# Performance work log

Hardware: AMD Instinct MI355X
Metric: run time of the kernel (lower is better)

The kernel has to match this reference:

```python
import jax, jax.numpy as jnp
import numpy as np

N = 50000   # nodes
E = 800000  # edges
F = 128     # input features
H = 128     # hidden channels
G = 64      # graphs in batch
C = 10      # classes
L_HID = 3   # residual hidden GCN blocks
EPS = 1e-5  # BatchNorm eps


def setup_inputs() -> dict:
    key = jax.random.key(0)
    ks = jax.random.split(key, 10)
    sc = lambda k, s: (jax.random.normal(k, s, jnp.float32) * 0.05)
    x = jax.random.normal(ks[0], (N, F), jnp.float32)
    edge_index = jax.random.randint(ks[1], (2, E), 0, N, dtype=jnp.int32)
    batch = jnp.sort(jax.random.randint(ks[2], (N,), 0, G, dtype=jnp.int32))
    return {
        "x": x, "edge_index": edge_index, "batch": batch,
        # initial GCN block
        "W0": sc(ks[3], (F, H)), "b0": jnp.zeros(H, jnp.float32),
        "g0": jnp.ones(H, jnp.float32), "be0": jnp.zeros(H, jnp.float32),
        # 3 residual GCN blocks (stacked)
        "Wh": sc(ks[4], (L_HID, H, H)), "bh": jnp.zeros((L_HID, H), jnp.float32),
        "gh": jnp.ones((L_HID, H), jnp.float32), "beh": jnp.zeros((L_HID, H), jnp.float32),
        "Rh": sc(ks[5], (L_HID, H, H)),  # residual Linear (no bias)
        # MLP head: Linear(H,H)+ReLU, Linear(H,C)
        "mW1": sc(ks[6], (H, H)), "mb1": jnp.zeros(H, jnp.float32),
        "mW2": sc(ks[7], (H, C)), "mb2": jnp.zeros(C, jnp.float32),
    }


def _gcn_norm(edge_index, n):
    # add self-loops + symmetric normalization, as in PyG GCNConv
    loop = jnp.arange(n, dtype=edge_index.dtype)
    src = jnp.concatenate([edge_index[0], loop])
    dst = jnp.concatenate([edge_index[1], loop])
    deg = jax.ops.segment_sum(jnp.ones_like(dst, jnp.float32), dst, num_segments=n)
    dinv = jnp.where(deg > 0, jax.lax.rsqrt(deg), 0.0)
    coef = dinv[src] * dinv[dst]  # [E+N]
    return src, dst, coef


def _gcn_conv(x, W, b, src, dst, coef, n):
    h = x @ W                                   # [N, H] linear first (PyG order)
    msg = h[src] * coef[:, None]                # gather + normalize  [E+N, H]
    agg = jax.ops.segment_sum(msg, dst, num_segments=n)  # scatter-add [N, H]
    return agg + b


def _bn_relu(h, gamma, beta):
    # BatchNorm1d in eval mode with running_mean=0, running_var=1
    inv = jax.lax.rsqrt(jnp.asarray(1.0 + EPS, h.dtype))
    return jax.nn.relu(h * inv * gamma + beta)  # dropout is identity in eval


def reference(x, edge_index, batch, W0, b0, g0, be0, Wh, bh, gh, beh, Rh, mW1, mb1, mW2, mb2):
    n = x.shape[0]
    src, dst, coef = _gcn_norm(edge_index, n)
    # initial block (no residual)
    h = _bn_relu(_gcn_conv(x, W0, b0, src, dst, coef, n), g0, be0)
    # residual hidden blocks
    for i in range(Wh.shape[0]):
        c = _gcn_conv(h, Wh[i], bh[i], src, dst, coef, n) + h @ Rh[i]
        h = _bn_relu(c, gh[i], beh[i])
    # global max pool over graphs in the batch
    pooled = jax.ops.segment_max(h, batch, num_segments=G)  # [G, H]
    # MLP head
    z = jax.nn.relu(pooled @ mW1 + mb1)
    return z @ mW2 + mb2  # [G, C]
```

## Files before the change

### kernel.cpp

```cpp
#include <hip/hip_runtime.h>
#include <cstdint>
#include <cstddef>

#define NN 50000
#define NE 800000
#define NEPAD (NE + 3 * NN)
#define HID 128
#define NGRAPH 64
#define NCLASS 10
#define LHID 3

#define ROWBLK 3125
#define ROWBLK_PAD 3128
#define GEMM_GRID 782
#define FILL_GRID 3125
#define FRONT_A 3125
#define FRONT_B 56
#define FRONT_GRID (FRONT_A + FRONT_B + 3125)

static constexpr float BN_INV = 0.9999950000374996f;

typedef __attribute__((ext_vector_type(8))) __bf16 bf16x8;
typedef __attribute__((ext_vector_type(4))) float floatx4;


__device__ __forceinline__ unsigned int f32_to_bf16_rne(float f) {
    unsigned int u = __float_as_uint(f);
    return (u + 0x7FFFu + ((u >> 16) & 1u)) >> 16;
}
__device__ __forceinline__ float bf16_to_f32(unsigned int h) {
    return __uint_as_float(h << 16);
}
__device__ __forceinline__ void split2(float a, float b, unsigned int& hi,
                                       unsigned int& lo) {
    unsigned int h0 = f32_to_bf16_rne(a), h1 = f32_to_bf16_rne(b);
    unsigned int l0 = f32_to_bf16_rne(a - bf16_to_f32(h0));
    unsigned int l1 = f32_to_bf16_rne(b - bf16_to_f32(h1));
    hi = h0 | (h1 << 16);
    lo = l0 | (l1 << 16);
}

__device__ __forceinline__ void gl2lds16(const void* g, void* l) {
    __builtin_amdgcn_global_load_lds((__attribute__((address_space(1))) void*)g,
                                     (__attribute__((address_space(3))) void*)l,
                                     16, 0, 0);
}


__global__ void k_front(const float* __restrict__ x, unsigned short* __restrict__ xH,
                        unsigned short* __restrict__ xL,
                        const float* __restrict__ W0, const float* __restrict__ Wh,
                        const float* __restrict__ Rh, unsigned short* __restrict__ bH,
                        unsigned short* __restrict__ bL,
                        const int* __restrict__ ei, int* __restrict__ deg,
                        int* __restrict__ eslot) {
    const int b = blockIdx.x;
    const int tid = threadIdx.x;
    if (b < FRONT_A) {
        int u = b * 256 + tid;
        int lane = u & 63;
        int blk = u >> 6;
        int kblk = blk & 3;
        int rowBlock = blk >> 2;
        int m = rowBlock * 16 + (lane & 15);
        int k = kblk * 32 + (lane >> 4) * 8;
        const float4* p = (const float4*)&x[(size_t)m * 128 + k];
        float4 v0 = p[0];
        float4 v1 = p[1];
        float vals[8] = {v0.x, v0.y, v0.z, v0.w, v1.x, v1.y, v1.z, v1.w};
        union { unsigned int i[4]; uint4 v; } H, L;
#pragma unroll
        for (int j = 0; j < 4; ++j) split2(vals[2 * j], vals[2 * j + 1], H.i[j], L.i[j]);
        *(uint4*)&xH[(size_t)u * 8] = H.v;
        *(uint4*)&xL[(size_t)u * 8] = L.v;
    } else if (b < FRONT_A + FRONT_B) {
        int cb = b - FRONT_A;
        int mat = cb >> 3;
        const float* src = (mat == 0) ? W0
                         : (mat <= 3) ? (Wh + (size_t)(mat - 1) * 16384)
                                      : (Rh + (size_t)(mat - 4) * 16384);
        int u = (cb & 7) * 256 + tid;
        int lane = u & 63;
        int blk = u >> 6;
        int kblk = blk & 3;
        int nb = blk >> 2;
        int n = nb * 16 + (lane & 15);
        int k = kblk * 32 + (lane >> 4) * 8;
        union { unsigned int i[4]; uint4 v; } H, L;
#pragma unroll
        for (int j = 0; j < 4; ++j) {
            float a = src[(size_t)(k + 2 * j) * 128 + n];
            float c = src[(size_t)(k + 2 * j + 1) * 128 + n];
            split2(a, c, H.i[j], L.i[j]);
        }
        size_t base = (size_t)mat * 16384 + (size_t)u * 8;
        *(uint4*)&bH[base] = H.v;
        *(uint4*)&bL[base] = L.v;
    } else {
        int e = (b - FRONT_A - FRONT_B) * 256 + tid;
        int d = ei[NE + e];
        eslot[e] = atomicAdd(&deg[d], 1);
    }
}


__global__ void k_scan1(const int* __restrict__ deg, float* __restrict__ dinv,
                        int* __restrict__ bsum) {
    __shared__ int s[256];
    int i = blockIdx.x * 256 + threadIdx.x;
    int d = (i < NN) ? deg[i] : 0;
    if (i < NN) dinv[i] = rsqrtf((float)(d + 1));
    s[threadIdx.x] = (d + 3) & ~3;
    __syncthreads();
    for (int o = 128; o > 0; o >>= 1) {
        if (threadIdx.x < o) s[threadIdx.x] += s[threadIdx.x + o];
        __syncthreads();
    }
    if (threadIdx.x == 0) bsum[blockIdx.x] = s[0];
}


__global__ void k_scan3(const int* __restrict__ deg, const int* __restrict__ bsum,
                        int* __restrict__ rowptr, int* __restrict__ col,
                        float* __restrict__ cfv) {
    __shared__ int s[256];
    __shared__ int offS;
    const int bid = blockIdx.x;
    s[threadIdx.x] = (threadIdx.x < bid) ? bsum[threadIdx.x] : 0;
    __syncthreads();
    for (int o = 128; o > 0; o >>= 1) {
        if (threadIdx.x < o) s[threadIdx.x] += s[threadIdx.x + o];
        __syncthreads();
    }
    if (threadIdx.x == 0) offS = s[0];
    __syncthreads();
    const int off = offS;
    __syncthreads();
    int i = bid * 256 + threadIdx.x;
    int d = (i < NN) ? deg[i] : 0;
    int v = (d + 3) & ~3;
    s[threadIdx.x] = v;
    __syncthreads();
    for (int o = 1; o < 256; o <<= 1) {
        int tv = (threadIdx.x >= o) ? s[threadIdx.x - o] : 0;
        __syncthreads();
        s[threadIdx.x] += tv;
        __syncthreads();
    }
    if (i < NN) {
        int rp = off + s[threadIdx.x] - v;
        rowptr[i] = rp;
        for (int p = rp + d; p < rp + v; ++p) { col[p] = 0; cfv[p] = 0.f; }
    }
}


template <int NB, bool FILL>
__global__ __launch_bounds__(256, 3) void k_gemm_mfma(
    const unsigned short* __restrict__ Ahi, const unsigned short* __restrict__ Alo,
    const unsigned short* __restrict__ B1hi, const unsigned short* __restrict__ B1lo,
    const unsigned short* __restrict__ B2hi, const unsigned short* __restrict__ B2lo,
    float* __restrict__ C1, float* __restrict__ C2,
    const int* __restrict__ ei, const int* __restrict__ rowptr,
    const int* __restrict__ eslot, const float* __restrict__ dinv,
    int* __restrict__ col, float* __restrict__ cfv) {
    __shared__ unsigned short lds[(1 + 2 * NB) * 4096];
    if (FILL && blockIdx.x >= GEMM_GRID) {
        int e = (blockIdx.x - GEMM_GRID) * 256 + threadIdx.x;
        int s = ei[e];
        int d = ei[NE + e];
        int p = rowptr[d] + eslot[e];
        col[p] = s;
        cfv[p] = dinv[s];
        return;
    }
    unsigned short* AhiS = lds;
    unsigned short* AloS = lds + 2048;
    unsigned short* B1hiS = lds + 4096;
    unsigned short* B1loS = lds + 8192;
    unsigned short* B2hiS = lds + 12288;
    unsigned short* B2loS = lds + 16384;

    const int tid = threadIdx.x;
    const int wave = tid >> 6;
    const int lane = tid & 63;
    const int wm = wave & 1;
    const int wn = wave >> 1;
    const int rb0 = blockIdx.x * 4;

    floatx4 acc1[2][4], acc2[2][4];
    floatx4 zero = {0.f, 0.f, 0.f, 0.f};
#pragma unroll
    for (int i = 0; i < 2; ++i)
#pragma unroll
        for (int j = 0; j < 4; ++j) { acc1[i][j] = zero; if (NB == 2) acc2[i][j] = zero; }

    for (int kc = 0; kc < 4; ++kc) {
        const int nit = (NB == 2) ? 10 : 6;
#pragma unroll
        for (int it = 0; it < nit; ++it) {
            int i = it * 4 + wave;
            const unsigned short* src;
            unsigned short* dst;
            if (i < 4)       { src = Ahi  + ((size_t)(rb0 + i) * 4 + kc) * 512;       dst = AhiS  + i * 512; }
            else if (i < 8)  { int rb = i - 4;  src = Alo  + ((size_t)(rb0 + rb) * 4 + kc) * 512; dst = AloS  + rb * 512; }
            else if (i < 16) { int nb = i - 8;  src = B1hi + ((size_t)nb * 4 + kc) * 512;         dst = B1hiS + nb * 512; }
            else if (i < 24) { int nb = i - 16; src = B1lo + ((size_t)nb * 4 + kc) * 512;         dst = B1loS + nb * 512; }
            else if (i < 32) { int nb = i - 24; src = B2hi + ((size_t)nb * 4 + kc) * 512;         dst = B2hiS + nb * 512; }
            else             { int nb = i - 32; src = B2lo + ((size_t)nb * 4 + kc) * 512;         dst = B2loS + nb * 512; }
            gl2lds16(src + (size_t)lane * 8, dst);
        }
        __syncthreads();

        bf16x8 aH[2], aL[2], bH[4], bL[4];
#pragma unroll
        for (int t = 0; t < 2; ++t)
            aH[t] = *(const bf16x8*)(AhiS + (wm * 2 + t) * 512 + lane * 8);
#pragma unroll
        for (int t = 0; t < 4; ++t)
            bH[t] = *(const bf16x8*)(B1hiS + (wn * 4 + t) * 512 + lane * 8);
#pragma unroll
        for (int tm = 0; tm < 2; ++tm)
#pragma unroll
            for (int tn = 0; tn < 4; ++tn)
                acc1[tm][tn] = __builtin_amdgcn_mfma_f32_16x16x32_bf16(
                    aH[tm], bH[tn], acc1[tm][tn], 0, 0, 0);
#pragma unroll
        for (int t = 0; t < 4; ++t)
            bL[t] = *(const bf16x8*)(B1loS + (wn * 4 + t) * 512 + lane * 8);
#pragma unroll
        for (int tm = 0; tm < 2; ++tm)
#pragma unroll
            for (int tn = 0; tn < 4; ++tn)
                acc1[tm][tn] = __builtin_amdgcn_mfma_f32_16x16x32_bf16(
                    aH[tm], bL[tn], acc1[tm][tn], 0, 0, 0);
#pragma unroll
        for (int t = 0; t < 2; ++t)
            aL[t] = *(const bf16x8*)(AloS + (wm * 2 + t) * 512 + lane * 8);
#pragma unroll
        for (int tm = 0; tm < 2; ++tm)
#pragma unroll
            for (int tn = 0; tn < 4; ++tn)
                acc1[tm][tn] = __builtin_amdgcn_mfma_f32_16x16x32_bf16(
                    aL[tm], bH[tn], acc1[tm][tn], 0, 0, 0);
        if (NB == 2) {
#pragma unroll
            for (int t = 0; t < 4; ++t)
                bH[t] = *(const bf16x8*)(B2hiS + (wn * 4 + t) * 512 + lane * 8);
#pragma unroll
            for (int tm = 0; tm < 2; ++tm)
#pragma unroll
                for (int tn = 0; tn < 4; ++tn)
                    acc2[tm][tn] = __builtin_amdgcn_mfma_f32_16x16x32_bf16(
                        aH[tm], bH[tn], acc2[tm][tn], 0, 0, 0);
#pragma unroll
            for (int tm = 0; tm < 2; ++tm)
#pragma unroll
                for (int tn = 0; tn < 4; ++tn)
                    acc2[tm][tn] = __builtin_amdgcn_mfma_f32_16x16x32_bf16(
                        aL[tm], bH[tn], acc2[tm][tn], 0, 0, 0);
#pragma unroll
            for (int t = 0; t < 4; ++t)
                bL[t] = *(const bf16x8*)(B2loS + (wn * 4 + t) * 512 + lane * 8);
#pragma unroll
            for (int tm = 0; tm < 2; ++tm)
#pragma unroll
                for (int tn = 0; tn < 4; ++tn)
                    acc2[tm][tn] = __builtin_amdgcn_mfma_f32_16x16x32_bf16(
                        aH[tm], bL[tn], acc2[tm][tn], 0, 0, 0);
        }
        __syncthreads();
    }

    const int quad = lane >> 4;
    const int col0 = lane & 15;
    const int rowBase = blockIdx.x * 64 + wm * 32;
#pragma unroll
    for (int tm = 0; tm < 2; ++tm) {
#pragma unroll
        for (int tn = 0; tn < 4; ++tn) {
            int c = wn * 64 + tn * 16 + col0;
#pragma unroll
            for (int r = 0; r < 4; ++r) {
                int row = rowBase + tm * 16 + quad * 4 + r;
                if (row < NN) {
                    C1[(size_t)row * 128 + c] = acc1[tm][tn][r];
                    if (NB == 2) C2[(size_t)row * 128 + c] = acc2[tm][tn][r];
                }
            }
        }
    }
}


template <bool RES, bool LAST>
__global__ __launch_bounds__(256) void k_spmm(const float* __restrict__ t,
                                              const float* __restrict__ r,
                                              const int* __restrict__ rowptr,
                                              const int* __restrict__ deg,
                                              const int* __restrict__ col,
                                              const float* __restrict__ cfv,
                                              const float* __restrict__ dinv,
                                              const float* __restrict__ bias,
                                              const float* __restrict__ gamma,
                                              const float* __restrict__ beta,
                                              unsigned short* __restrict__ hHi,
                                              unsigned short* __restrict__ hLo,
                                              const int* __restrict__ batch,
                                              float* __restrict__ pooled) {
    __shared__ unsigned short shH[16][136];
    __shared__ unsigned short shL[16][136];
    const int lane = threadIdx.x & 63;
    const int wave = threadIdx.x >> 6;
    const int f = lane * 2;
    const float2 bv = *(const float2*)&bias[f];
    const float2 gv = *(const float2*)&gamma[f];
    const float2 ev = *(const float2*)&beta[f];

    int curg = -1;
    float mx = 0.f, my = 0.f;

#pragma unroll 1
    for (int i = 0; i < 4; ++i) {
        const int nl = wave * 4 + i;
        const int node = blockIdx.x * 16 + nl;
        const int start = rowptr[node];
        const int cnt4 = (deg[node] + 3) >> 2;
        float ax = 0.f, ay = 0.f;
#pragma unroll 2
        for (int q = 0; q < cnt4; ++q) {
            int4 cs = *(const int4*)&col[start + q * 4];
            float4 wv = *(const float4*)&cfv[start + q * 4];
            float2 v0 = *(const float2*)&t[(size_t)cs.x * 128 + f];
            float2 v1 = *(const float2*)&t[(size_t)cs.y * 128 + f];
            float2 v2 = *(const float2*)&t[(size_t)cs.z * 128 + f];
            float2 v3 = *(const float2*)&t[(size_t)cs.w * 128 + f];
            ax = fmaf(wv.x, v0.x, ax); ay = fmaf(wv.x, v0.y, ay);
            ax = fmaf(wv.y, v1.x, ax); ay = fmaf(wv.y, v1.y, ay);
            ax = fmaf(wv.z, v2.x, ax); ay = fmaf(wv.z, v2.y, ay);
            ax = fmaf(wv.w, v3.x, ax); ay = fmaf(wv.w, v3.y, ay);
        }
        const float di = dinv[node];
        const float dii = di * di;
        float2 tv = *(const float2*)&t[(size_t)node * 128 + f];
        float cx = di * ax + dii * tv.x + bv.x;
        float cy = di * ay + dii * tv.y + bv.y;
        if (RES) {
            float2 rv = *(const float2*)&r[(size_t)node * 128 + f];
            cx += rv.x;
            cy += rv.y;
        }
        float ox = fmaxf(cx * (BN_INV * gv.x) + ev.x, 0.f);
        float oy = fmaxf(cy * (BN_INV * gv.y) + ev.y, 0.f);
        if (LAST) {
            int g = batch[node];
            if (g != curg) {
                if (curg >= 0) {
                    atomicMax((unsigned int*)&pooled[curg * 128 + f], __float_as_uint(mx));
                    atomicMax((unsigned int*)&pooled[curg * 128 + f + 1], __float_as_uint(my));
                }
                curg = g; mx = ox; my = oy;
            } else {
                mx = fmaxf(mx, ox);
                my = fmaxf(my, oy);
            }
        } else {
            unsigned int H, L;
            split2(ox, oy, H, L);
            ((unsigned int*)&shH[nl][0])[lane] = H;
            ((unsigned int*)&shL[nl][0])[lane] = L;
        }
    }

    if (LAST) {
        if (curg >= 0) {
            atomicMax((unsigned int*)&pooled[curg * 128 + f], __float_as_uint(mx));
            atomicMax((unsigned int*)&pooled[curg * 128 + f + 1], __float_as_uint(my));
        }
        return;
    }
    __syncthreads();

    const int u = threadIdx.x >> 6;
    const int l = threadIdx.x & 63;
    const int m = l & 15;
    const int kg = l >> 4;
    uint4 H4 = *(const uint4*)&shH[m][u * 32 + kg * 8];
    uint4 L4 = *(const uint4*)&shL[m][u * 32 + kg * 8];
    ((uint4*)hHi)[((size_t)blockIdx.x * 4 + u) * 64 + l] = H4;
    ((uint4*)hLo)[((size_t)blockIdx.x * 4 + u) * 64 + l] = L4;
}


__global__ void k_head(const float* __restrict__ pooled, const float* __restrict__ mW1,
                       const float* __restrict__ mb1, const float* __restrict__ mW2,
                       const float* __restrict__ mb2, float* __restrict__ out) {
    __shared__ float p[128];
    __shared__ float z[128];
    int g = blockIdx.x;
    int j = threadIdx.x;
    p[j] = pooled[g * 128 + j];
    __syncthreads();
    float a = mb1[j];
#pragma unroll 8
    for (int k = 0; k < 128; ++k) a += p[k] * mW1[k * 128 + j];
    z[j] = fmaxf(a, 0.f);
    __syncthreads();
    if (j < NCLASS) {
        float o = mb2[j];
#pragma unroll 8
        for (int k = 0; k < 128; ++k) o += z[k] * mW2[k * NCLASS + j];
        out[g * NCLASS + j] = o;
    }
}


extern "C" void kernel_launch(void* const* d_in, const int* in_sizes, int n_in,
                              void* d_out, int out_size, void* d_ws, size_t ws_size,
                              hipStream_t stream) {
    const float* x   = (const float*)d_in[0];
    const int*   ei  = (const int*)d_in[1];
    const int* batch = (const int*)d_in[2];
    const float* W0  = (const float*)d_in[3];
    const float* b0  = (const float*)d_in[4];
    const float* g0  = (const float*)d_in[5];
    const float* be0 = (const float*)d_in[6];
    const float* Wh  = (const float*)d_in[7];
    const float* bh  = (const float*)d_in[8];
    const float* gh  = (const float*)d_in[9];
    const float* beh = (const float*)d_in[10];
    const float* Rh  = (const float*)d_in[11];
    const float* mW1 = (const float*)d_in[12];
    const float* mb1 = (const float*)d_in[13];
    const float* mW2 = (const float*)d_in[14];
    const float* mb2 = (const float*)d_in[15];
    float* out = (float*)d_out;

    char* ws = (char*)d_ws;
    size_t off = 0;
    auto alloc = [&](size_t bytes) -> void* {
        void* p = ws + off;
        off += (bytes + 255) & ~(size_t)255;
        return p;
    };
    int*   deg    = (int*)alloc((size_t)NN * 4);
    float* pooled = (float*)alloc((size_t)NGRAPH * HID * 4);
    size_t zspan = (size_t)((char*)pooled - (char*)deg) + (size_t)NGRAPH * HID * 4;
    int*   rowptr = (int*)alloc((size_t)NN * 4);
    float* dinv   = (float*)alloc((size_t)NN * 4);
    int*   bsum   = (int*)alloc(256 * 4);
    int*   eslot  = (int*)alloc((size_t)NE * 4);
    int*   col    = (int*)alloc((size_t)NEPAD * 4);
    float* cfv    = (float*)alloc((size_t)NEPAD * 4);
    float* t      = (float*)alloc((size_t)NN * HID * 4);
    float* rbuf   = (float*)alloc((size_t)NN * HID * 4);
    const size_t ASZ = (size_t)ROWBLK_PAD * 4 * 512;
    unsigned short* xH = (unsigned short*)alloc(ASZ * 2);
    unsigned short* xL = (unsigned short*)alloc(ASZ * 2);
    unsigned short* hH0 = (unsigned short*)alloc(ASZ * 2);
    unsigned short* hL0 = (unsigned short*)alloc(ASZ * 2);
    unsigned short* hH1 = (unsigned short*)alloc(ASZ * 2);
    unsigned short* hL1 = (unsigned short*)alloc(ASZ * 2);
    unsigned short* bH = (unsigned short*)alloc((size_t)7 * 16384 * 2);
    unsigned short* bL = (unsigned short*)alloc((size_t)7 * 16384 * 2);

    hipMemsetAsync(deg, 0, zspan, stream);

    k_front<<<FRONT_GRID, 256, 0, stream>>>(x, xH, xL, W0, Wh, Rh, bH, bL,
                                            ei, deg, eslot);
    k_scan1<<<(NN + 255) / 256, 256, 0, stream>>>(deg, dinv, bsum);
    k_scan3<<<(NN + 255) / 256, 256, 0, stream>>>(deg, bsum, rowptr, col, cfv);

    k_gemm_mfma<1, true><<<GEMM_GRID + FILL_GRID, 256, 0, stream>>>(
        xH, xL, bH, bL, nullptr, nullptr, t, nullptr,
        ei, rowptr, eslot, dinv, col, cfv);

    const int spmmGrid = NN / 16;
    k_spmm<false, false><<<spmmGrid, 256, 0, stream>>>(
        t, nullptr, rowptr, deg, col, cfv, dinv, b0, g0, be0, hH0, hL0,
        nullptr, nullptr);

    unsigned short* hh[2] = {hH0, hH1};
    unsigned short* hl[2] = {hL0, hL1};
    int cur = 0;
    for (int i = 0; i < LHID; ++i) {
        unsigned short* ih = hh[cur];
        unsigned short* il = hl[cur];
        unsigned short* oh = hh[cur ^ 1];
        unsigned short* ol = hl[cur ^ 1];
        const unsigned short* w1H = bH + (size_t)(1 + i) * 16384;
        const unsigned short* w1L = bL + (size_t)(1 + i) * 16384;
        const unsigned short* w2H = bH + (size_t)(4 + i) * 16384;
        const unsigned short* w2L = bL + (size_t)(4 + i) * 16384;
        k_gemm_mfma<2, false><<<GEMM_GRID, 256, 0, stream>>>(
            ih, il, w1H, w1L, w2H, w2L, t, rbuf,
            nullptr, nullptr, nullptr, nullptr, nullptr, nullptr);
        if (i < LHID - 1)
            k_spmm<true, false><<<spmmGrid, 256, 0, stream>>>(
                t, rbuf, rowptr, deg, col, cfv, dinv, bh + i * HID, gh + i * HID,
                beh + i * HID, oh, ol, nullptr, nullptr);
        else
            k_spmm<true, true><<<spmmGrid, 256, 0, stream>>>(
                t, rbuf, rowptr, deg, col, cfv, dinv, bh + i * HID, gh + i * HID,
                beh + i * HID, nullptr, nullptr, batch, pooled);
        cur ^= 1;
    }

    k_head<<<NGRAPH, 128, 0, stream>>>(pooled, mW1, mb1, mW2, mb2, out);
}
```

Baseline: 526.3 us.

## Fuse MLP head into last SpMM via last-block counter and uniform-graph pooling

Removes the separate head kernel launch: the last block of the final SpMM, found with an atomic completion counter, runs the MLP head over all pooled graphs. Blocks whose 16 nodes all belong to one graph first reduce their max in shared memory, so only wave 0 issues the atomicMax calls. The gather loop unroll also goes from 2 to 4. The cost is a serialized tail, where a single block computes the whole head, plus extra shared memory and sync barriers in the last SpMM.

```diff
diff --git a/kernel.cpp b/kernel.cpp
--- a/kernel.cpp
+++ b/kernel.cpp
@@ -307,9 +307,19 @@
                                               unsigned short* __restrict__ hHi,
                                               unsigned short* __restrict__ hLo,
                                               const int* __restrict__ batch,
-                                              float* __restrict__ pooled) {
+                                              float* __restrict__ pooled,
+                                              int* __restrict__ counter,
+                                              const float* __restrict__ mW1,
+                                              const float* __restrict__ mb1,
+                                              const float* __restrict__ mW2,
+                                              const float* __restrict__ mb2,
+                                              float* __restrict__ out) {
     __shared__ unsigned short shH[16][136];
     __shared__ unsigned short shL[16][136];
+    __shared__ float shP[4][64][2];
+    __shared__ float shPool[2][128];
+    __shared__ float shZ[2][128];
+    __shared__ int shDone;
     const int lane = threadIdx.x & 63;
     const int wave = threadIdx.x >> 6;
     const int f = lane * 2;
@@ -317,6 +327,8 @@
     const float2 gv = *(const float2*)&gamma[f];
     const float2 ev = *(const float2*)&beta[f];
 
+    bool uni = false;
+    if (LAST) uni = (batch[blockIdx.x * 16] == batch[blockIdx.x * 16 + 15]);
     int curg = -1;
     float mx = 0.f, my = 0.f;
 
@@ -327,7 +339,7 @@
         const int start = rowptr[node];
         const int cnt4 = (deg[node] + 3) >> 2;
         float ax = 0.f, ay = 0.f;
-#pragma unroll 2
+#pragma unroll 4
         for (int q = 0; q < cnt4; ++q) {
             int4 cs = *(const int4*)&col[start + q * 4];
             float4 wv = *(const float4*)&cfv[start + q * 4];
@@ -353,16 +365,21 @@
         float ox = fmaxf(cx * (BN_INV * gv.x) + ev.x, 0.f);
         float oy = fmaxf(cy * (BN_INV * gv.y) + ev.y, 0.f);
         if (LAST) {
-            int g = batch[node];
-            if (g != curg) {
-                if (curg >= 0) {
-                    atomicMax((unsigned int*)&pooled[curg * 128 + f], __float_as_uint(mx));
-                    atomicMax((unsigned int*)&pooled[curg * 128 + f + 1], __float_as_uint(my));
-                }
-                curg = g; mx = ox; my = oy;
-            } else {
+            if (uni) {
                 mx = fmaxf(mx, ox);
                 my = fmaxf(my, oy);
+            } else {
+                int g = batch[node];
+                if (g != curg) {
+                    if (curg >= 0) {
+                        atomicMax((unsigned int*)&pooled[curg * 128 + f], __float_as_uint(mx));
+                        atomicMax((unsigned int*)&pooled[curg * 128 + f + 1], __float_as_uint(my));
+                    }
+                    curg = g; mx = ox; my = oy;
+                } else {
+                    mx = fmaxf(mx, ox);
+                    my = fmaxf(my, oy);
+                }
             }
         } else {
             unsigned int H, L;
@@ -373,9 +390,54 @@
     }
 
     if (LAST) {
-        if (curg >= 0) {
-            atomicMax((unsigned int*)&pooled[curg * 128 + f], __float_as_uint(mx));
-            atomicMax((unsigned int*)&pooled[curg * 128 + f + 1], __float_as_uint(my));
+        if (uni) {
+            shP[wave][lane][0] = mx;
+            shP[wave][lane][1] = my;
+            __syncthreads();
+            if (wave == 0) {
+                int g = batch[blockIdx.x * 16];
+                float a = fmaxf(fmaxf(shP[0][lane][0], shP[1][lane][0]),
+                                fmaxf(shP[2][lane][0], shP[3][lane][0]));
+                float b = fmaxf(fmaxf(shP[0][lane][1], shP[1][lane][1]),
+                                fmaxf(shP[2][lane][1], shP[3][lane][1]));
+                atomicMax((unsigned int*)&pooled[g * 128 + f], __float_as_uint(a));
+                atomicMax((unsigned int*)&pooled[g * 128 + f + 1], __float_as_uint(b));
+            }
+        } else {
+            if (curg >= 0) {
+                atomicMax((unsigned int*)&pooled[curg * 128 + f], __float_as_uint(mx));
+                atomicMax((unsigned int*)&pooled[curg * 128 + f + 1], __float_as_uint(my));
+            }
+        }
+        __syncthreads();
+        if (threadIdx.x == 0) {
+            __threadfence();
+            shDone = atomicAdd(counter, 1);
+        }
+        __syncthreads();
+        if (shDone == (int)gridDim.x - 1) {
+            const int j = threadIdx.x & 127;
+            const int half = threadIdx.x >> 7;
+            for (int g0 = 0; g0 < NGRAPH; g0 += 2) {
+                int idx = threadIdx.x;
+                shPool[idx >> 7][idx & 127] = __uint_as_float(
+                    atomicMax((unsigned int*)&pooled[(g0 + (idx >> 7)) * 128 + (idx & 127)], 0u));
+                __syncthreads();
+                float a = mb1[j];
+#pragma unroll 8
+                for (int k = 0; k < 128; ++k)
+                    a = fmaf(shPool[half][k], mW1[k * 128 + j], a);
+                shZ[half][j] = fmaxf(a, 0.f);
+                __syncthreads();
+                if (j < NCLASS) {
+                    float o = mb2[j];
+#pragma unroll 8
+                    for (int k = 0; k < 128; ++k)
+                        o = fmaf(shZ[half][k], mW2[k * NCLASS + j], o);
+                    out[(g0 + half) * NCLASS + j] = o;
+                }
+                __syncthreads();
+            }
         }
         return;
     }
@@ -389,29 +451,6 @@
     uint4 L4 = *(const uint4*)&shL[m][u * 32 + kg * 8];
     ((uint4*)hHi)[((size_t)blockIdx.x * 4 + u) * 64 + l] = H4;
     ((uint4*)hLo)[((size_t)blockIdx.x * 4 + u) * 64 + l] = L4;
-}
-
-
-__global__ void k_head(const float* __restrict__ pooled, const float* __restrict__ mW1,
-                       const float* __restrict__ mb1, const float* __restrict__ mW2,
-                       const float* __restrict__ mb2, float* __restrict__ out) {
-    __shared__ float p[128];
-    __shared__ float z[128];
-    int g = blockIdx.x;
-    int j = threadIdx.x;
-    p[j] = pooled[g * 128 + j];
-    __syncthreads();
-    float a = mb1[j];
-#pragma unroll 8
-    for (int k = 0; k < 128; ++k) a += p[k] * mW1[k * 128 + j];
-    z[j] = fmaxf(a, 0.f);
-    __syncthreads();
-    if (j < NCLASS) {
-        float o = mb2[j];
-#pragma unroll 8
-        for (int k = 0; k < 128; ++k) o += z[k] * mW2[k * NCLASS + j];
-        out[g * NCLASS + j] = o;
-    }
 }
 
 
@@ -443,9 +482,10 @@
         off += (bytes + 255) & ~(size_t)255;
         return p;
     };
-    int*   deg    = (int*)alloc((size_t)NN * 4);
-    float* pooled = (float*)alloc((size_t)NGRAPH * HID * 4);
-    size_t zspan = (size_t)((char*)pooled - (char*)deg) + (size_t)NGRAPH * HID * 4;
+    int*   deg     = (int*)alloc((size_t)NN * 4);
+    float* pooled  = (float*)alloc((size_t)NGRAPH * HID * 4);
+    int*   counter = (int*)alloc(256);
+    size_t zspan = (size_t)((char*)counter - (char*)deg) + 256;
     int*   rowptr = (int*)alloc((size_t)NN * 4);
     float* dinv   = (float*)alloc((size_t)NN * 4);
     int*   bsum   = (int*)alloc(256 * 4);
@@ -478,7 +518,7 @@
     const int spmmGrid = NN / 16;
     k_spmm<false, false><<<spmmGrid, 256, 0, stream>>>(
         t, nullptr, rowptr, deg, col, cfv, dinv, b0, g0, be0, hH0, hL0,
-        nullptr, nullptr);
+        nullptr, nullptr, nullptr, nullptr, nullptr, nullptr, nullptr, nullptr);
 
     unsigned short* hh[2] = {hH0, hH1};
     unsigned short* hl[2] = {hL0, hL1};
@@ -498,13 +538,13 @@
         if (i < LHID - 1)
             k_spmm<true, false><<<spmmGrid, 256, 0, stream>>>(
                 t, rbuf, rowptr, deg, col, cfv, dinv, bh + i * HID, gh + i * HID,
-                beh + i * HID, oh, ol, nullptr, nullptr);
+                beh + i * HID, oh, ol, nullptr, nullptr, nullptr,
+                nullptr, nullptr, nullptr, nullptr, nullptr);
         else
             k_spmm<true, true><<<spmmGrid, 256, 0, stream>>>(
                 t, rbuf, rowptr, deg, col, cfv, dinv, bh + i * HID, gh + i * HID,
-                beh + i * HID, nullptr, nullptr, batch, pooled);
+                beh + i * HID, nullptr, nullptr, batch, pooled, counter,
+                mW1, mb1, mW2, mb2, out);
         cur ^= 1;
     }
-
-    k_head<<<NGRAPH, 128, 0, stream>>>(pooled, mW1, mb1, mW2, mb2, out);
-}
+}
```

After: 757.6 us. +44.0%, slower.

## Use one wave per node in SpMM with 1024-thread blocks and block-level pooling

Applied to the files above, without the earlier changes.

The SpMM kernel now runs 16 waves per block, with each wave aggregating exactly one node, where before 4 waves each looped over 4 nodes sequentially. This exposes more independent gather streams to hide memory latency. In the last layer, blocks whose 16 nodes all belong to one graph reduce the max through shared memory before a single set of atomics. Other blocks issue per-node atomics, which costs more atomic traffic at graph boundaries. The larger blocks may limit occupancy granularity and raise register pressure under the 1024-thread launch bound.

```diff
diff --git a/kernel.cpp b/kernel.cpp
--- a/kernel.cpp
+++ b/kernel.cpp
@@ -294,101 +294,104 @@
 
 
 template <bool RES, bool LAST>
-__global__ __launch_bounds__(256) void k_spmm(const float* __restrict__ t,
-                                              const float* __restrict__ r,
-                                              const int* __restrict__ rowptr,
-                                              const int* __restrict__ deg,
-                                              const int* __restrict__ col,
-                                              const float* __restrict__ cfv,
-                                              const float* __restrict__ dinv,
-                                              const float* __restrict__ bias,
-                                              const float* __restrict__ gamma,
-                                              const float* __restrict__ beta,
-                                              unsigned short* __restrict__ hHi,
-                                              unsigned short* __restrict__ hLo,
-                                              const int* __restrict__ batch,
-                                              float* __restrict__ pooled) {
+__global__ __launch_bounds__(1024) void k_spmm(const float* __restrict__ t,
+                                               const float* __restrict__ r,
+                                               const int* __restrict__ rowptr,
+                                               const int* __restrict__ deg,
+                                               const int* __restrict__ col,
+                                               const float* __restrict__ cfv,
+                                               const float* __restrict__ dinv,
+                                               const float* __restrict__ bias,
+                                               const float* __restrict__ gamma,
+                                               const float* __restrict__ beta,
+                                               unsigned short* __restrict__ hHi,
+                                               unsigned short* __restrict__ hLo,
+                                               const int* __restrict__ batch,
+                                               float* __restrict__ pooled) {
     __shared__ unsigned short shH[16][136];
     __shared__ unsigned short shL[16][136];
+    __shared__ float shP[16][64][2];
     const int lane = threadIdx.x & 63;
     const int wave = threadIdx.x >> 6;
     const int f = lane * 2;
+    const int node = blockIdx.x * 16 + wave;
+
     const float2 bv = *(const float2*)&bias[f];
     const float2 gv = *(const float2*)&gamma[f];
     const float2 ev = *(const float2*)&beta[f];
 
-    int curg = -1;
-    float mx = 0.f, my = 0.f;
-
-#pragma unroll 1
-    for (int i = 0; i < 4; ++i) {
-        const int nl = wave * 4 + i;
-        const int node = blockIdx.x * 16 + nl;
-        const int start = rowptr[node];
-        const int cnt4 = (deg[node] + 3) >> 2;
-        float ax = 0.f, ay = 0.f;
+    const int start = rowptr[node];
+    const int cnt4 = (deg[node] + 3) >> 2;
+    float ax = 0.f, ay = 0.f;
 #pragma unroll 2
-        for (int q = 0; q < cnt4; ++q) {
-            int4 cs = *(const int4*)&col[start + q * 4];
-            float4 wv = *(const float4*)&cfv[start + q * 4];
-            float2 v0 = *(const float2*)&t[(size_t)cs.x * 128 + f];
-            float2 v1 = *(const float2*)&t[(size_t)cs.y * 128 + f];
-            float2 v2 = *(const float2*)&t[(size_t)cs.z * 128 + f];
-            float2 v3 = *(const float2*)&t[(size_t)cs.w * 128 + f];
-            ax = fmaf(wv.x, v0.x, ax); ay = fmaf(wv.x, v0.y, ay);
-            ax = fmaf(wv.y, v1.x, ax); ay = fmaf(wv.y, v1.y, ay);
-            ax = fmaf(wv.z, v2.x, ax); ay = fmaf(wv.z, v2.y, ay);
-            ax = fmaf(wv.w, v3.x, ax); ay = fmaf(wv.w, v3.y, ay);
-        }
-        const float di = dinv[node];
-        const float dii = di * di;
-        float2 tv = *(const float2*)&t[(size_t)node * 128 + f];
-        float cx = di * ax + dii * tv.x + bv.x;
-        float cy = di * ay + dii * tv.y + bv.y;
-        if (RES) {
-            float2 rv = *(const float2*)&r[(size_t)node * 128 + f];
-            cx += rv.x;
-            cy += rv.y;
-        }
-        float ox = fmaxf(cx * (BN_INV * gv.x) + ev.x, 0.f);
-        float oy = fmaxf(cy * (BN_INV * gv.y) + ev.y, 0.f);
-        if (LAST) {
-            int g = batch[node];
-            if (g != curg) {
-                if (curg >= 0) {
-                    atomicMax((unsigned int*)&pooled[curg * 128 + f], __float_as_uint(mx));
-                    atomicMax((unsigned int*)&pooled[curg * 128 + f + 1], __float_as_uint(my));
+    for (int q = 0; q < cnt4; ++q) {
+        int4 cs = *(const int4*)&col[start + q * 4];
+        float4 wv = *(const float4*)&cfv[start + q * 4];
+        float2 v0 = *(const float2*)&t[(size_t)cs.x * 128 + f];
+        float2 v1 = *(const float2*)&t[(size_t)cs.y * 128 + f];
+        float2 v2 = *(const float2*)&t[(size_t)cs.z * 128 + f];
+        float2 v3 = *(const float2*)&t[(size_t)cs.w * 128 + f];
+        ax = fmaf(wv.x, v0.x, ax); ay = fmaf(wv.x, v0.y, ay);
+        ax = fmaf(wv.y, v1.x, ax); ay = fmaf(wv.y, v1.y, ay);
+        ax = fmaf(wv.z, v2.x, ax); ay = fmaf(wv.z, v2.y, ay);
+        ax = fmaf(wv.w, v3.x, ax); ay = fmaf(wv.w, v3.y, ay);
+    }
+    const float di = dinv[node];
+    const float dii = di * di;
+    float2 tv = *(const float2*)&t[(size_t)node * 128 + f];
+    float cx = di * ax + dii * tv.x + bv.x;
+    float cy = di * ay + dii * tv.y + bv.y;
+    if (RES) {
+        float2 rv = *(const float2*)&r[(size_t)node * 128 + f];
+        cx += rv.x;
+        cy += rv.y;
+    }
+    const float ox = fmaxf(cx * (BN_INV * gv.x) + ev.x, 0.f);
+    const float oy = fmaxf(cy * (BN_INV * gv.y) + ev.y, 0.f);
+
+    if (LAST) {
+        bool uni = (batch[blockIdx.x * 16] == batch[blockIdx.x * 16 + 15]);
+        if (uni) {
+            shP[wave][lane][0] = ox;
+            shP[wave][lane][1] = oy;
+            __syncthreads();
+            if (wave == 0) {
+                float a = shP[0][lane][0], b = shP[0][lane][1];
+#pragma unroll
+                for (int w = 1; w < 16; ++w) {
+                    a = fmaxf(a, shP[w][lane][0]);
+                    b = fmaxf(b, shP[w][lane][1]);
                 }
-                curg = g; mx = ox; my = oy;
-            } else {
-                mx = fmaxf(mx, ox);
-                my = fmaxf(my, oy);
+                int g = batch[blockIdx.x * 16];
+                atomicMax((unsigned int*)&pooled[g * 128 + f], __float_as_uint(a));
+                atomicMax((unsigned int*)&pooled[g * 128 + f + 1], __float_as_uint(b));
             }
         } else {
-            unsigned int H, L;
-            split2(ox, oy, H, L);
-            ((unsigned int*)&shH[nl][0])[lane] = H;
-            ((unsigned int*)&shL[nl][0])[lane] = L;
-        }
-    }
-
-    if (LAST) {
-        if (curg >= 0) {
-            atomicMax((unsigned int*)&pooled[curg * 128 + f], __float_as_uint(mx));
-            atomicMax((unsigned int*)&pooled[curg * 128 + f + 1], __float_as_uint(my));
+            int g = batch[node];
+            atomicMax((unsigned int*)&pooled[g * 128 + f], __float_as_uint(ox));
+            atomicMax((unsigned int*)&pooled[g * 128 + f + 1], __float_as_uint(oy));
         }
         return;
     }
+
+    unsigned int H, L;
+    split2(ox, oy, H, L);
+    ((unsigned int*)&shH[wave][0])[lane] = H;
+    ((unsigned int*)&shL[wave][0])[lane] = L;
     __syncthreads();
 
     const int u = threadIdx.x >> 6;
     const int l = threadIdx.x & 63;
     const int m = l & 15;
     const int kg = l >> 4;
-    uint4 H4 = *(const uint4*)&shH[m][u * 32 + kg * 8];
-    uint4 L4 = *(const uint4*)&shL[m][u * 32 + kg * 8];
-    ((uint4*)hHi)[((size_t)blockIdx.x * 4 + u) * 64 + l] = H4;
-    ((uint4*)hLo)[((size_t)blockIdx.x * 4 + u) * 64 + l] = L4;
+    if (u < 4) {
+        uint4 H4 = *(const uint4*)&shH[m][u * 32 + kg * 8];
+        ((uint4*)hHi)[((size_t)blockIdx.x * 4 + u) * 64 + l] = H4;
+    } else if (u < 8) {
+        int uu = u - 4;
+        uint4 L4 = *(const uint4*)&shL[m][uu * 32 + kg * 8];
+        ((uint4*)hLo)[((size_t)blockIdx.x * 4 + uu) * 64 + l] = L4;
+    }
 }
 
 
@@ -476,7 +479,7 @@
         ei, rowptr, eslot, dinv, col, cfv);
 
     const int spmmGrid = NN / 16;
-    k_spmm<false, false><<<spmmGrid, 256, 0, stream>>>(
+    k_spmm<false, false><<<spmmGrid, 1024, 0, stream>>>(
         t, nullptr, rowptr, deg, col, cfv, dinv, b0, g0, be0, hH0, hL0,
         nullptr, nullptr);
 
@@ -496,11 +499,11 @@
             ih, il, w1H, w1L, w2H, w2L, t, rbuf,
             nullptr, nullptr, nullptr, nullptr, nullptr, nullptr);
         if (i < LHID - 1)
-            k_spmm<true, false><<<spmmGrid, 256, 0, stream>>>(
+            k_spmm<true, false><<<spmmGrid, 1024, 0, stream>>>(
                 t, rbuf, rowptr, deg, col, cfv, dinv, bh + i * HID, gh + i * HID,
                 beh + i * HID, oh, ol, nullptr, nullptr);
         else
-            k_spmm<true, true><<<spmmGrid, 256, 0, stream>>>(
+            k_spmm<true, true><<<spmmGrid, 1024, 0, stream>>>(
                 t, rbuf, rowptr, deg, col, cfv, dinv, bh + i * HID, gh + i * HID,
                 beh + i * HID, nullptr, nullptr, batch, pooled);
         cur ^= 1;
```

New measurement: 509.5 us. -3.2%, faster.
